# Optimization experiments

Measured on AMD Instinct MI355X. Metric: run time of the kernel, lower is better.

## Reference

```python
import jax, jax.numpy as jnp
import numpy as np

N = 500_000          # number of particles
D = 6                # phase-space dimension
N_BINS = 128         # bins per axis
SQRT2 = 1.4142135623730951
BANDWIDTH = 1.0      # kernel width relative to bin width (module default)


def setup_inputs() -> dict:
    key = jax.random.key(0)
    x = jax.random.normal(key, (N, D), dtype=jnp.float32)
    edges = jnp.linspace(-3.0, 3.0, N_BINS + 1, dtype=jnp.float32)
    return {"x": x, "bin_edges_x": edges, "bin_edges_y": edges}


def _cdf_weights(u, edges, bw):
    """Per-point Gaussian mass in each bin via CDF (erf) differences.

    u: (n,), edges: (m+1,) -> weights (n, m); row sums <= 1.
    """
    z = jax.scipy.special.erf((edges[None, :] - u[:, None]) / (bw * SQRT2))  # (n, m+1)
    return 0.5 * (z[:, 1:] - z[:, :-1])  # (n, m)


def reference(x, bin_edges_x, bin_edges_y):
    dx = bin_edges_x[1] - bin_edges_x[0]
    dy = bin_edges_y[1] - bin_edges_y[0]
    bw_x = BANDWIDTH * dx
    bw_y = BANDWIDTH * dy
    # axis = (0, 1): project onto first two phase-space coordinates
    wx = _cdf_weights(x[:, 0], bin_edges_x, bw_x)  # (n, bx)
    wy = _cdf_weights(x[:, 1], bin_edges_y, bw_y)  # (n, by)
    hist = jnp.einsum('ni,nj->ij', wx, wy)         # (bx, by)
    # normalize to a probability density over the grid
    hist = hist / (hist.sum() * dx * dy)
    return hist
```

## Files before the change

kernel.cpp:

```cpp
#include <hip/hip_runtime.h>
#include <math.h>


#define NBINS   128
#define NB2     (NBINS * NBINS)
#define KC      256
#define AX_B    32768
#define THREADS 512
#define NBLOCKS 512
#define NGRP    16
#define PPG     (NBLOCKS / NGRP)
#define QSCALE  320.0f

typedef int i32x4 __attribute__((ext_vector_type(4)));

__global__ __launch_bounds__(THREADS, 4) void hist_mfma_kernel(
    const float* __restrict__ x,
    const float* __restrict__ edges_x,
    const float* __restrict__ edges_y,
    float* __restrict__ partials,
    float* __restrict__ btot,
    int n)
{
    __shared__ __align__(16) signed char sh[2 * AX_B];
    __shared__ int xw[8];

    const int tid  = threadIdx.x;
    const int lane = tid & 63;
    const int wv   = tid >> 6;

    const float e0x = edges_x[0];
    const float dxw = edges_x[1] - e0x;
    const float e0y = edges_y[0];
    const float dyw = edges_y[1] - e0y;

    const int axis = tid >> 8;
    const int pl   = tid & 255;
    const float e0   = axis ? e0y : e0x;
    const float invd = 1.0f / (axis ? dyw : dxw);
    const float cc   = 0.7071067811865476f;
    signed char* const sdst =
        sh + axis * AX_B + (pl >> 6) * 1024 + ((pl >> 4) & 3) * 256 + (pl & 15);

    i32x4 acc[4][4];
    #pragma unroll
    for (int i = 0; i < 4; ++i)
        #pragma unroll
        for (int j = 0; j < 4; ++j)
            acc[i][j] = (i32x4){0, 0, 0, 0};

    const int rowQ = ((wv >> 1) & 1) * 4;
    const int colQ = (wv & 1) * 4;
    const int ks0  = (wv >> 2) * 2;

    const int nchunks = (n + KC - 1) / KC;
    for (int chunk = blockIdx.x; chunk < nchunks; chunk += gridDim.x) {
        const int p = chunk * KC + pl;
        float u = 1e30f;
        if (p < n) u = x[(size_t)p * 6 + axis];

        const float spos = (u - e0) * invd;
        int b0 = (int)floorf(spos + 0.5f) - 4;
        b0 = b0 < 0 ? 0 : (b0 > NBINS - 8 ? NBINS - 8 : b0);
        const float t0 = ((float)b0 - spos) * cc;
        float z[9];
        #pragma unroll
        for (int k = 0; k < 9; ++k) z[k] = erff(t0 + (float)k * cc);
        signed char qv[8];
        #pragma unroll
        for (int k = 0; k < 8; ++k)
            qv[k] = (signed char)(int)rintf(0.5f * (z[k + 1] - z[k]) * QSCALE);

        float4* zp = (float4*)sh;
        #pragma unroll
        for (int i = 0; i < 8; ++i)
            zp[tid + i * THREADS] = (float4){0.f, 0.f, 0.f, 0.f};
        __syncthreads();

        #pragma unroll
        for (int k = 0; k < 8; ++k) {
            const int b = b0 + k;
            sdst[(b >> 4) * 4096 + (b & 15) * 16] = qv[k];
        }
        __syncthreads();

        #pragma unroll
        for (int s = 0; s < 2; ++s) {
            const int ks = ks0 + s;
            i32x4 av[4], bv[4];
            #pragma unroll
            for (int i = 0; i < 4; ++i)
                av[i] = *(const i32x4*)(sh + (rowQ + i) * 4096 + ks * 1024 + lane * 16);
            #pragma unroll
            for (int j = 0; j < 4; ++j)
                bv[j] = *(const i32x4*)(sh + AX_B + (colQ + j) * 4096 + ks * 1024 + lane * 16);
            #pragma unroll
            for (int i = 0; i < 4; ++i)
                #pragma unroll
                for (int j = 0; j < 4; ++j)
                    acc[i][j] = __builtin_amdgcn_mfma_i32_16x16x64_i8(
                        av[i], bv[j], acc[i][j], 0, 0, 0);
        }
        __syncthreads();
    }

    if (wv >= 4) {
        int* dst = (int*)sh + (wv - 4) * 4096;
        #pragma unroll
        for (int i = 0; i < 4; ++i)
            #pragma unroll
            for (int j = 0; j < 4; ++j)
                #pragma unroll
                for (int g = 0; g < 4; ++g)
                    dst[((i * 4 + j) * 4 + g) * 64 + lane] = acc[i][j][g];
    }
    __syncthreads();

    int bsum = 0;
    if (wv < 4) {
        const float qs = 1.0f / (QSCALE * QSCALE);
        const int* src = (const int*)sh + wv * 4096;
        float* my = partials + (size_t)blockIdx.x * NB2;
        const int r0 = (lane >> 4) * 4;
        const int c0 = lane & 15;
        #pragma unroll
        for (int i = 0; i < 4; ++i)
            #pragma unroll
            for (int j = 0; j < 4; ++j)
                #pragma unroll
                for (int g = 0; g < 4; ++g) {
                    const int v = acc[i][j][g] + src[((i * 4 + j) * 4 + g) * 64 + lane];
                    bsum += v;
                    const int row = (rowQ + i) * 16 + r0 + g;
                    const int col = (colQ + j) * 16 + c0;
                    my[row * NBINS + col] = (float)v * qs;
                }
    }
    #pragma unroll
    for (int off = 32; off > 0; off >>= 1) bsum += __shfl_down(bsum, off, 64);
    if (lane == 0) xw[wv] = bsum;
    __syncthreads();
    if (tid == 0) {
        const float qs = 1.0f / (QSCALE * QSCALE);
        btot[blockIdx.x] = (float)(xw[0] + xw[1] + xw[2] + xw[3]) * qs;
    }
}

__global__ void reduceA_kernel(const float* __restrict__ partials,
                               float* __restrict__ partial2)
{
    const int bin4 = (blockIdx.x * 256 + threadIdx.x) * 4;
    const int g = blockIdx.y;
    const float4* p = (const float4*)(partials + (size_t)g * PPG * NB2 + bin4);
    float4 s = {0.f, 0.f, 0.f, 0.f};
    #pragma unroll
    for (int k = 0; k < PPG; ++k) {
        const float4 v = p[(size_t)k * (NB2 / 4)];
        s.x += v.x; s.y += v.y; s.z += v.z; s.w += v.w;
    }
    *(float4*)(partial2 + (size_t)g * NB2 + bin4) = s;
}

__global__ void scaleB_kernel(const float* __restrict__ partial2,
                              const float* __restrict__ btot,
                              const float* __restrict__ edges_x,
                              const float* __restrict__ edges_y,
                              float* __restrict__ out)
{
    __shared__ float ws[4];
    __shared__ float stot;

    float t = 0.0f;
    for (int i = threadIdx.x; i < NBLOCKS; i += 256) t += btot[i];
    #pragma unroll
    for (int off = 32; off > 0; off >>= 1) t += __shfl_down(t, off, 64);
    if ((threadIdx.x & 63) == 0) ws[threadIdx.x >> 6] = t;
    __syncthreads();
    if (threadIdx.x == 0) {
        const float dxw = edges_x[1] - edges_x[0];
        const float dyw = edges_y[1] - edges_y[0];
        stot = 1.0f / ((ws[0] + ws[1] + ws[2] + ws[3]) * dxw * dyw);
    }
    __syncthreads();

    const int bin = blockIdx.x * blockDim.x + threadIdx.x;
    float s = 0.0f;
    #pragma unroll
    for (int g = 0; g < NGRP; ++g) s += partial2[g * NB2 + bin];
    out[bin] = s * stot;
}

extern "C" void kernel_launch(void* const* d_in, const int* in_sizes, int n_in,
                              void* d_out, int out_size, void* d_ws, size_t ws_size,
                              hipStream_t stream)
{
    const float* x  = (const float*)d_in[0];
    const float* ex = (const float*)d_in[1];
    const float* ey = (const float*)d_in[2];
    float* out = (float*)d_out;
    const int n = in_sizes[0] / 6;

    float* partials = (float*)d_ws;
    float* partial2 = partials + (size_t)NBLOCKS * NB2;
    float* btot     = partial2 + (size_t)NGRP * NB2;

    hist_mfma_kernel<<<NBLOCKS, THREADS, 0, stream>>>(x, ex, ey, partials, btot, n);
    reduceA_kernel<<<dim3(NB2 / 1024, NGRP), 256, 0, stream>>>(partials, partial2);
    scaleB_kernel<<<NB2 / 256, 256, 0, stream>>>(partial2, btot, ex, ey, out);
}
```

Measured before the change: 89.17 us.

## Store partial histograms as bf16, fuse reductions, prefetch next chunk's weights

Per-block partial histograms are now written as bf16 instead of fp32, which halves the workspace traffic. The two reduction kernels are merged into a single kernel that sums all 512 partials per bin tile and applies the normalization, removing one launch and the intermediate buffer. In the main loop, the next chunk's input load and erf/quantize work now happen after the MFMA step, so they overlap with matrix work. The cost is bf16 rounding error in the partials before they are summed.

```diff
diff --git a/kernel.cpp b/kernel.cpp
--- a/kernel.cpp
+++ b/kernel.cpp
@@ -8,17 +8,24 @@
 #define AX_B    32768
 #define THREADS 512
 #define NBLOCKS 512
-#define NGRP    16
-#define PPG     (NBLOCKS / NGRP)
 #define QSCALE  320.0f
 
 typedef int i32x4 __attribute__((ext_vector_type(4)));
+
+static __device__ __forceinline__ unsigned short f2bf(float f) {
+    unsigned int b = __float_as_uint(f);
+    b += 0x7fff + ((b >> 16) & 1);
+    return (unsigned short)(b >> 16);
+}
+static __device__ __forceinline__ float bf2f(unsigned short u) {
+    return __uint_as_float((unsigned int)u << 16);
+}
 
 __global__ __launch_bounds__(THREADS, 4) void hist_mfma_kernel(
     const float* __restrict__ x,
     const float* __restrict__ edges_x,
     const float* __restrict__ edges_y,
-    float* __restrict__ partials,
+    unsigned short* __restrict__ partials,
     float* __restrict__ btot,
     int n)
 {
@@ -54,22 +61,34 @@
     const int ks0  = (wv >> 2) * 2;
 
     const int nchunks = (n + KC - 1) / KC;
-    for (int chunk = blockIdx.x; chunk < nchunks; chunk += gridDim.x) {
-        const int p = chunk * KC + pl;
-        float u = 1e30f;
-        if (p < n) u = x[(size_t)p * 6 + axis];
-
+
+    float u = 1e30f;
+    {
+        const int p = blockIdx.x * KC + pl;
+        if (blockIdx.x < nchunks && p < n) u = x[(size_t)p * 6 + axis];
+    }
+    int b0;
+    signed char qv[8];
+    {
         const float spos = (u - e0) * invd;
-        int b0 = (int)floorf(spos + 0.5f) - 4;
-        b0 = b0 < 0 ? 0 : (b0 > NBINS - 8 ? NBINS - 8 : b0);
+        int b = (int)floorf(spos + 0.5f) - 4;
+        b0 = b < 0 ? 0 : (b > NBINS - 8 ? NBINS - 8 : b);
         const float t0 = ((float)b0 - spos) * cc;
         float z[9];
         #pragma unroll
         for (int k = 0; k < 9; ++k) z[k] = erff(t0 + (float)k * cc);
-        signed char qv[8];
         #pragma unroll
         for (int k = 0; k < 8; ++k)
             qv[k] = (signed char)(int)rintf(0.5f * (z[k + 1] - z[k]) * QSCALE);
+    }
+
+    for (int chunk = blockIdx.x; chunk < nchunks; chunk += gridDim.x) {
+        const int nchunk = chunk + gridDim.x;
+        float un = 1e30f;
+        if (nchunk < nchunks) {
+            const int pn = nchunk * KC + pl;
+            if (pn < n) un = x[(size_t)pn * 6 + axis];
+        }
 
         float4* zp = (float4*)sh;
         #pragma unroll
@@ -101,6 +120,19 @@
                     acc[i][j] = __builtin_amdgcn_mfma_i32_16x16x64_i8(
                         av[i], bv[j], acc[i][j], 0, 0, 0);
         }
+
+        {
+            const float spos = (un - e0) * invd;
+            int b = (int)floorf(spos + 0.5f) - 4;
+            b0 = b < 0 ? 0 : (b > NBINS - 8 ? NBINS - 8 : b);
+            const float t0 = ((float)b0 - spos) * cc;
+            float z[9];
+            #pragma unroll
+            for (int k = 0; k < 9; ++k) z[k] = erff(t0 + (float)k * cc);
+            #pragma unroll
+            for (int k = 0; k < 8; ++k)
+                qv[k] = (signed char)(int)rintf(0.5f * (z[k + 1] - z[k]) * QSCALE);
+        }
         __syncthreads();
     }
 
@@ -120,7 +152,7 @@
     if (wv < 4) {
         const float qs = 1.0f / (QSCALE * QSCALE);
         const int* src = (const int*)sh + wv * 4096;
-        float* my = partials + (size_t)blockIdx.x * NB2;
+        unsigned short* my = partials + (size_t)blockIdx.x * NB2;
         const int r0 = (lane >> 4) * 4;
         const int c0 = lane & 15;
         #pragma unroll
@@ -133,7 +165,7 @@
                     bsum += v;
                     const int row = (rowQ + i) * 16 + r0 + g;
                     const int col = (colQ + j) * 16 + c0;
-                    my[row * NBINS + col] = (float)v * qs;
+                    my[row * NBINS + col] = f2bf((float)v * qs);
                 }
     }
     #pragma unroll
@@ -146,48 +178,54 @@
     }
 }
 
-__global__ void reduceA_kernel(const float* __restrict__ partials,
-                               float* __restrict__ partial2)
-{
-    const int bin4 = (blockIdx.x * 256 + threadIdx.x) * 4;
-    const int g = blockIdx.y;
-    const float4* p = (const float4*)(partials + (size_t)g * PPG * NB2 + bin4);
-    float4 s = {0.f, 0.f, 0.f, 0.f};
-    #pragma unroll
-    for (int k = 0; k < PPG; ++k) {
-        const float4 v = p[(size_t)k * (NB2 / 4)];
-        s.x += v.x; s.y += v.y; s.z += v.z; s.w += v.w;
-    }
-    *(float4*)(partial2 + (size_t)g * NB2 + bin4) = s;
-}
-
-__global__ void scaleB_kernel(const float* __restrict__ partial2,
+__global__ void reduce_kernel(const unsigned short* __restrict__ partials,
                               const float* __restrict__ btot,
                               const float* __restrict__ edges_x,
                               const float* __restrict__ edges_y,
                               float* __restrict__ out)
 {
+    __shared__ float4 red[8][32];
     __shared__ float ws[4];
     __shared__ float stot;
 
-    float t = 0.0f;
-    for (int i = threadIdx.x; i < NBLOCKS; i += 256) t += btot[i];
+    const int t = threadIdx.x;
+    const int bin4 = t & 31;
+    const int pg = t >> 5;
+    const int binBase = blockIdx.x * 128;
+
+    float tl = btot[t] + btot[t + 256];
     #pragma unroll
-    for (int off = 32; off > 0; off >>= 1) t += __shfl_down(t, off, 64);
-    if ((threadIdx.x & 63) == 0) ws[threadIdx.x >> 6] = t;
-    __syncthreads();
-    if (threadIdx.x == 0) {
+    for (int off = 32; off > 0; off >>= 1) tl += __shfl_down(tl, off, 64);
+    if ((t & 63) == 0) ws[t >> 6] = tl;
+
+    const unsigned short* p =
+        partials + (size_t)(pg * 64) * NB2 + binBase + bin4 * 4;
+    float4 s = {0.f, 0.f, 0.f, 0.f};
+    #pragma unroll 8
+    for (int k = 0; k < 64; ++k) {
+        const ushort4 v = *(const ushort4*)(p + (size_t)k * NB2);
+        s.x += bf2f(v.x); s.y += bf2f(v.y); s.z += bf2f(v.z); s.w += bf2f(v.w);
+    }
+    red[pg][bin4] = s;
+    __syncthreads();
+
+    if (t == 0) {
         const float dxw = edges_x[1] - edges_x[0];
         const float dyw = edges_y[1] - edges_y[0];
         stot = 1.0f / ((ws[0] + ws[1] + ws[2] + ws[3]) * dxw * dyw);
     }
     __syncthreads();
 
-    const int bin = blockIdx.x * blockDim.x + threadIdx.x;
-    float s = 0.0f;
-    #pragma unroll
-    for (int g = 0; g < NGRP; ++g) s += partial2[g * NB2 + bin];
-    out[bin] = s * stot;
+    if (t < 32) {
+        float4 a = red[0][t];
+        #pragma unroll
+        for (int g = 1; g < 8; ++g) {
+            const float4 b = red[g][t];
+            a.x += b.x; a.y += b.y; a.z += b.z; a.w += b.w;
+        }
+        a.x *= stot; a.y *= stot; a.z *= stot; a.w *= stot;
+        *(float4*)(out + binBase + t * 4) = a;
+    }
 }
 
 extern "C" void kernel_launch(void* const* d_in, const int* in_sizes, int n_in,
@@ -200,11 +238,9 @@
     float* out = (float*)d_out;
     const int n = in_sizes[0] / 6;
 
-    float* partials = (float*)d_ws;
-    float* partial2 = partials + (size_t)NBLOCKS * NB2;
-    float* btot     = partial2 + (size_t)NGRP * NB2;
+    unsigned short* partials = (unsigned short*)d_ws;
+    float* btot = (float*)((char*)d_ws + (size_t)NBLOCKS * NB2 * 2);
 
     hist_mfma_kernel<<<NBLOCKS, THREADS, 0, stream>>>(x, ex, ey, partials, btot, n);
-    reduceA_kernel<<<dim3(NB2 / 1024, NGRP), 256, 0, stream>>>(partials, partial2);
-    scaleB_kernel<<<NB2 / 256, 256, 0, stream>>>(partial2, btot, ex, ey, out);
-}
+    reduce_kernel<<<NB2 / 128, 256, 0, stream>>>(partials, btot, ex, ey, out);
+}
```

Result: no change. 89.89 us (+0.8%).
